# Kernel tuning notes

Measured on AMD Instinct MI355X. Metric: run time of the kernel, lower is better.

The kernel has to match this reference:

```python
import jax, jax.numpy as jnp
from jax import lax
import numpy as np

B, W, D = 32, 256, 512      # batch, input_window, d_model == feature_size
NHID = W // 2               # GAT hidden per head = 128
NHEADS = 4
ALPHA = 0.1                 # LeakyReLU slope (GAT default)
NEG = -1e9                  # masked-softmax fill


def conv1d(x, w, b):
    # x: [B, C, L], w: [O, I, K=3], 'same' padding, stride 1
    y = lax.conv_general_dilated(x, w, (1,), 'SAME', dimension_numbers=('NCH', 'OIH', 'NCH'))
    return y + b[None, :, None]


def gat_heads(h, adj, Wt, bb, ai, ai_b, aj, aj_b):
    # h: [B, N, F_in], adj: [B, N, N]; vectorized over NHEADS heads
    Wh = jnp.einsum('bnf,hof->bhno', h, Wt) + bb[None, :, None, :]   # [B,H,N,NHID]
    e1 = jnp.einsum('bhno,ho->bhn', Wh, ai) + ai_b[None, :, None]
    e2 = jnp.einsum('bhno,ho->bhn', Wh, aj) + aj_b[None, :, None]
    e = jax.nn.leaky_relu(e1[..., :, None] + e2[..., None, :], ALPHA)  # [B,H,N,N]
    att = jax.nn.softmax(jnp.where(adj[:, None] > 0, e, NEG), axis=-1)
    return jnp.einsum('bhnm,bhmo->bhno', att, Wh)


def gat_out(h, adj, Wt, bb, ai, ai_b, aj, aj_b):
    # h: [B, N, NHEADS*NHID] -> [B, N, W]
    Wh = h @ Wt.T + bb
    e1 = Wh @ ai + ai_b
    e2 = Wh @ aj + aj_b
    e = jax.nn.leaky_relu(e1[:, :, None] + e2[:, None, :], ALPHA)
    att = jax.nn.softmax(jnp.where(adj > 0, e, NEG), axis=-1)
    return jnp.einsum('bnm,bmo->bno', att, Wh)


def setup_inputs() -> dict:
    key = jax.random.key(0)
    ks = jax.random.split(key, 16)
    f32 = jnp.float32
    def xu(k, shape, fan_in):
        return jax.random.normal(k, shape, f32) * (1.414 / np.sqrt(fan_in))
    return {
        'x': jax.random.normal(ks[0], (B, W, D), f32),
        'qW': xu(ks[1], (D, D, 3), 3 * D), 'qb': jnp.zeros((D,), f32),
        'kW': xu(ks[2], (D, D, 3), 3 * D), 'kb': jnp.zeros((D,), f32),
        'vW': xu(ks[3], (D, D, 3), 3 * D), 'vb': jnp.zeros((D,), f32),
        'head_W': xu(ks[4], (NHEADS, NHID, W), W), 'head_b': jnp.zeros((NHEADS, NHID), f32),
        'head_ai': xu(ks[5], (NHEADS, NHID), NHID), 'head_ai_b': jnp.zeros((NHEADS,), f32),
        'head_aj': xu(ks[6], (NHEADS, NHID), NHID), 'head_aj_b': jnp.zeros((NHEADS,), f32),
        'out_W': xu(ks[7], (W, NHEADS * NHID), NHEADS * NHID), 'out_b': jnp.zeros((W,), f32),
        'out_ai': xu(ks[8], (W,), W), 'out_ai_b': jnp.zeros((), f32),
        'out_aj': xu(ks[9], (W,), W), 'out_aj_b': jnp.zeros((), f32),
        'proj_W': xu(ks[10], (D, D), D), 'proj_b': jnp.zeros((D,), f32),
    }


def reference(x, qW, qb, kW, kb, vW, vb,
              head_W, head_b, head_ai, head_ai_b, head_aj, head_aj_b,
              out_W, out_b, out_ai, out_ai_b, out_aj, out_aj_b,
              proj_W, proj_b):
    b, w, f = x.shape
    xt = jnp.transpose(x, (0, 2, 1))                 # [B, D, W]
    q = conv1d(xt, qW, qb)
    k = conv1d(xt, kW, kb)
    v = conv1d(xt, vW, vb)
    scale = 1.0 / jnp.sqrt(jnp.asarray(f, x.dtype))  # q.shape[-2] == d_model
    adj = jax.nn.sigmoid(jnp.einsum('bdw,bew->bde', q, k) * scale)  # [B, D, D]
    # GAT: nodes = feature dims (N=D), node features = window (W); dropout skipped (eval)
    hh = jax.nn.elu(gat_heads(v, adj, head_W, head_b, head_ai, head_ai_b, head_aj, head_aj_b))
    hcat = jnp.transpose(hh, (0, 2, 1, 3)).reshape(b, f, NHEADS * NHID)  # [B, D, 4*NHID]
    g = gat_out(hcat, adj, out_W, out_b, out_ai, out_ai_b, out_aj, out_aj_b)
    gat_y = jax.nn.log_softmax(jax.nn.elu(g), axis=2)  # [B, D, W]
    out = jnp.transpose(gat_y, (0, 2, 1)) @ proj_W.T + proj_b  # [B, W, D]
    return (out, adj)
```

## Files before the change

kernel.cpp:

```cpp
#include <hip/hip_runtime.h>
#include <math.h>

typedef unsigned short u16;
typedef __attribute__((ext_vector_type(8))) short short8;
typedef __attribute__((ext_vector_type(4))) float f32x4;

#define BB 32
#define WW 256
#define DD 512
#define NHEADS 4
#define NHID 128

__device__ __forceinline__ u16 f2bf(float f) {
  union { float f; unsigned int i; } x; x.f = f;
  unsigned int i = x.i;
  i += 0x7fffu + ((i >> 16) & 1u);
  return (u16)(i >> 16);
}
__device__ __forceinline__ float bf2f(u16 u) {
  union { float f; unsigned int i; } x; x.i = ((unsigned int)u) << 16; return x.f;
}

union BF8 { short8 v; u16 u[8]; };
union BF4 { ushort4 v; u16 u[4]; };
union F8 { float4 v4[2]; float f[8]; };

__global__ __launch_bounds__(256) void kprep_w(
    const float* __restrict__ qW, const float* __restrict__ kW, const float* __restrict__ vW,
    u16* __restrict__ Wt)
{
  int idx = blockIdx.x*256 + threadIdx.x;
  if (idx >= 3*DD*DD) return;
  int c = idx >> 18;
  int oi = idx & (DD*DD - 1);
  int i = oi & (DD-1);
  int o = oi >> 9;
  const float* W = (c==0) ? qW : (c==1) ? kW : vW;
  float w0 = W[oi*3+0], w1 = W[oi*3+1], w2 = W[oi*3+2];
  Wt[((size_t)(c*3+0)*DD + o)*DD + i] = f2bf(w0);
  Wt[((size_t)(c*3+1)*DD + o)*DD + i] = f2bf(w1);
  Wt[((size_t)(c*3+2)*DD + o)*DD + i] = f2bf(w2);
}

__global__ __launch_bounds__(256) void kcvt(const float* __restrict__ s, u16* __restrict__ d, int n) {
  int i = blockIdx.x*256 + threadIdx.x;
  if (i < n) d[i] = f2bf(s[i]);
}

__global__ __launch_bounds__(256) void kprep_a(
    const float* __restrict__ hW, const float* __restrict__ hai, const float* __restrict__ haib,
    const float* __restrict__ haj, const float* __restrict__ hajb,
    const float* __restrict__ hb,
    const float* __restrict__ oW, const float* __restrict__ oai, const float* __restrict__ oaib,
    const float* __restrict__ oaj, const float* __restrict__ oajb,
    const float* __restrict__ ob,
    float* __restrict__ ahat_i, float* __restrict__ ahat_j,
    float* __restrict__ oahat_i, float* __restrict__ oahat_j,
    float* __restrict__ cvec)
{
  int idx = blockIdx.x*256 + threadIdx.x;
  if (idx < 1024) {
    int h = idx >> 8, f = idx & 255;
    float s = 0.f;
    for (int o = 0; o < NHID; ++o) s += hW[((size_t)h*NHID + o)*WW + f] * hai[h*NHID + o];
    ahat_i[idx] = s;
  } else if (idx < 2048) {
    int t = idx - 1024; int h = t >> 8, f = t & 255;
    float s = 0.f;
    for (int o = 0; o < NHID; ++o) s += hW[((size_t)h*NHID + o)*WW + f] * haj[h*NHID + o];
    ahat_j[t] = s;
  } else if (idx < 2560) {
    int f = idx - 2048;
    float s = 0.f;
    for (int o = 0; o < WW; ++o) s += oW[(size_t)o*DD + f] * oai[o];
    oahat_i[f] = s;
  } else if (idx < 3072) {
    int f = idx - 2560;
    float s = 0.f;
    for (int o = 0; o < WW; ++o) s += oW[(size_t)o*DD + f] * oaj[o];
    oahat_j[f] = s;
  } else if (idx < 3082) {
    int t = idx - 3072;
    if (t < 4) {
      float s = 0.f;
      for (int o = 0; o < NHID; ++o) s += hb[t*NHID + o]*hai[t*NHID + o];
      cvec[t] = s + haib[t];
    } else if (t < 8) {
      int h = t - 4; float s = 0.f;
      for (int o = 0; o < NHID; ++o) s += hb[h*NHID + o]*haj[h*NHID + o];
      cvec[t] = s + hajb[h];
    } else if (t == 8) {
      float s = 0.f;
      for (int o = 0; o < WW; ++o) s += ob[o]*oai[o];
      cvec[8] = s + oaib[0];
    } else {
      float s = 0.f;
      for (int o = 0; o < WW; ++o) s += ob[o]*oaj[o];
      cvec[9] = s + oajb[0];
    }
  }
}

__global__ __launch_bounds__(256) void kprep_x(
    const float* __restrict__ x, int zb, int nrow8, u16* __restrict__ xpad)
{
  int idx8 = blockIdx.x*256 + threadIdx.x;
  if (idx8 >= nrow8) return;
  int i8 = idx8 & 63;
  int rowg = idx8 >> 6;
  int z = rowg / 258, r = rowg - z*258;
  int t = r - 1;
  BF8 o8;
  if (t >= 0 && t < WW) {
    const float* src = x + ((size_t)(zb+z)*WW + t)*DD + i8*8;
    float4 v0 = *reinterpret_cast<const float4*>(src);
    float4 v1 = *reinterpret_cast<const float4*>(src + 4);
    o8.u[0]=f2bf(v0.x); o8.u[1]=f2bf(v0.y); o8.u[2]=f2bf(v0.z); o8.u[3]=f2bf(v0.w);
    o8.u[4]=f2bf(v1.x); o8.u[5]=f2bf(v1.y); o8.u[6]=f2bf(v1.z); o8.u[7]=f2bf(v1.w);
  } else {
    #pragma unroll
    for (int j = 0; j < 8; ++j) o8.u[j] = 0;
  }
  *reinterpret_cast<short8*>(xpad + (size_t)rowg*DD + i8*8) = o8.v;
}

__global__ __launch_bounds__(256) void kexp2(
    const float* __restrict__ e2, float* __restrict__ M2,
    float* __restrict__ E2p, float* __restrict__ E2n)
{
  __shared__ float s4[4];
  const int zh = blockIdx.x, tid = threadIdx.x;
  float v0 = e2[(size_t)zh*DD + tid], v1 = e2[(size_t)zh*DD + 256 + tid];
  float m = fmaxf(v0, v1);
  #pragma unroll
  for (int off=32; off>=1; off>>=1) m = fmaxf(m, __shfl_xor(m, off));
  if ((tid & 63) == 0) s4[tid >> 6] = m;
  __syncthreads();
  m = fmaxf(fmaxf(s4[0], s4[1]), fmaxf(s4[2], s4[3]));
  if (tid == 0) M2[zh] = m;
  E2p[(size_t)zh*DD + tid]       = expf(v0 - m);
  E2p[(size_t)zh*DD + 256 + tid] = expf(v1 - m);
  E2n[(size_t)zh*DD + tid]       = expf(0.1f*(v0 - m));
  E2n[(size_t)zh*DD + 256 + tid] = expf(0.1f*(v1 - m));
}

__global__ __launch_bounds__(256) void k1_mfma(
    const u16* __restrict__ xpad, const u16* __restrict__ Wt,
    const float* __restrict__ qb, const float* __restrict__ kb, const float* __restrict__ vb,
    u16* __restrict__ qbf, u16* __restrict__ kbf, u16* __restrict__ vbf)
{
  __shared__ u16 bt[2][130*64];
  const int tid = threadIdx.x;
  const int w  = tid >> 6;
  const int l  = tid & 63;
  const int ln = l & 15;
  const int kg = l >> 4;
  const int og = blockIdx.x * 64 + w * 16;
  const int t0 = blockIdx.y * 128;
  const int z  = blockIdx.z;

  const u16* A0 = Wt + (size_t)(og + ln)*DD + kg*8;
  const u16* Xb = xpad + ((size_t)z*258 + t0)*DD;

  f32x4 acc[3][8];
  #pragma unroll
  for (int c=0;c<3;++c)
    #pragma unroll
    for (int ts=0;ts<8;++ts) acc[c][ts] = (f32x4){0.f,0.f,0.f,0.f};

  short8 ArP[9], ArQ[9];
  short8 sg0, sg1, sg2, sg3, sg4;
  const int ccw = tid & 7;
  const int rs = tid >> 3;

#define K1_LOADX(i0v) do { \
    sg0 = *reinterpret_cast<const short8*>(Xb + (size_t)rs*DD + (i0v) + ccw*8); \
    sg1 = *reinterpret_cast<const short8*>(Xb + (size_t)(rs+32)*DD + (i0v) + ccw*8); \
    sg2 = *reinterpret_cast<const short8*>(Xb + (size_t)(rs+64)*DD + (i0v) + ccw*8); \
    sg3 = *reinterpret_cast<const short8*>(Xb + (size_t)(rs+96)*DD + (i0v) + ccw*8); \
    if (tid < 16) sg4 = *reinterpret_cast<const short8*>(Xb + (size_t)(rs+128)*DD + (i0v) + ccw*8); \
  } while(0)

#define K1_WRITEX(bufv) do { \
    *reinterpret_cast<short8*>(&bt[bufv][rs*64 + ((ccw^(rs&7))<<3)]) = sg0; \
    *reinterpret_cast<short8*>(&bt[bufv][(rs+32)*64 + ((ccw^((rs+32)&7))<<3)]) = sg1; \
    *reinterpret_cast<short8*>(&bt[bufv][(rs+64)*64 + ((ccw^((rs+64)&7))<<3)]) = sg2; \
    *reinterpret_cast<short8*>(&bt[bufv][(rs+96)*64 + ((ccw^((rs+96)&7))<<3)]) = sg3; \
    if (tid < 16) *reinterpret_cast<short8*>(&bt[bufv][(rs+128)*64 + ((ccw^((rs+128)&7))<<3)]) = sg4; \
  } while(0)

#define K1_LOADA(Abuf, i0v, khv) do { \
    _Pragma("unroll") \
    for (int c = 0; c < 3; ++c) { \
      _Pragma("unroll") \
      for (int tap = 0; tap < 3; ++tap) \
        Abuf[c*3+tap] = *reinterpret_cast<const short8*>(A0 + (size_t)(c*3+tap)*DD*DD + (i0v) + (khv)*32); \
    } \
  } while(0)

#define K1_MFMAS(Abuf, khv) do { \
    _Pragma("unroll") \
    for (int tap = 0; tap < 3; ++tap) { \
      _Pragma("unroll") \
      for (int ts = 0; ts < 8; ++ts) { \
        int row = ts*16 + ln + tap; \
        short8 bfr = *reinterpret_cast<const short8*>(&bt[cur][row*64 + ((((khv)*4+kg) ^ (row&7))<<3)]); \
        acc[0][ts] = __builtin_amdgcn_mfma_f32_16x16x32_bf16(Abuf[0*3+tap], bfr, acc[0][ts], 0,0,0); \
        acc[1][ts] = __builtin_amdgcn_mfma_f32_16x16x32_bf16(Abuf[1*3+tap], bfr, acc[1][ts], 0,0,0); \
        acc[2][ts] = __builtin_amdgcn_mfma_f32_16x16x32_bf16(Abuf[2*3+tap], bfr, acc[2][ts], 0,0,0); \
      } \
    } \
  } while(0)

  K1_LOADX(0);
  K1_LOADA(ArP, 0, 0);
  K1_WRITEX(0);
  __syncthreads();

  int cur = 0;
  #pragma unroll 1
  for (int p = 0; p < 8; ++p) {
    const int i0 = p*64;
    if (p < 7) K1_LOADX(i0 + 64);
    K1_LOADA(ArQ, i0, 1);
    K1_MFMAS(ArP, 0);
    const int i0n = (p < 7) ? i0 + 64 : 0;
    K1_LOADA(ArP, i0n, 0);
    K1_MFMAS(ArQ, 1);
    if (p < 7) {
      K1_WRITEX(cur ^ 1);
      __syncthreads();
      cur ^= 1;
    }
  }

#undef K1_LOADX
#undef K1_WRITEX
#undef K1_LOADA
#undef K1_MFMAS

  #pragma unroll
  for (int ts=0; ts<8; ++ts) {
    int tg = t0 + ts*16 + ln;
    #pragma unroll
    for (int r=0;r<4;++r) {
      int o = og + kg*4 + r;
      size_t oi = (size_t)(z*DD + o)*WW + tg;
      qbf[oi] = f2bf(acc[0][ts][r] + qb[o]);
      kbf[oi] = f2bf(acc[1][ts][r] + kb[o]);
      vbf[oi] = f2bf(acc[2][ts][r] + vb[o]);
    }
  }
}

__global__ __launch_bounds__(256) void k2_adj(
    const u16* __restrict__ qbf, const u16* __restrict__ kbf, int zb, float* __restrict__ adjo)
{
  __shared__ u16 bp[2][64*64];
  const int tid = threadIdx.x;
  const int w = tid >> 6, l = tid & 63, ln = l & 15, kg = l >> 4;
  const int d0 = blockIdx.x*64 + w*16;
  const int e0 = blockIdx.y*64;
  const int z  = blockIdx.z;
  const int sc = tid & 7, sr = tid >> 3;
  const int sp = sc ^ (sr & 7);
  const int sp2 = sc ^ ((sr+32) & 7);
  const u16* B0 = kbf + (size_t)(z*DD + e0)*WW;
  const u16* Asrc = qbf + (size_t)(z*DD + d0 + ln)*WW + kg*8;

  f32x4 acc[4];
  #pragma unroll
  for (int es=0;es<4;++es) acc[es] = (f32x4){0.f,0.f,0.f,0.f};
  short8 aP0, aP1, aQ0, aQ1, sg0, sg1;

  sg0 = *reinterpret_cast<const short8*>(B0 + (size_t)sr*WW + sc*8);
  sg1 = *reinterpret_cast<const short8*>(B0 + (size_t)(sr+32)*WW + sc*8);
  aP0 = *reinterpret_cast<const short8*>(Asrc);
  aP1 = *reinterpret_cast<const short8*>(Asrc + 32);
  *reinterpret_cast<short8*>(&bp[0][sr*64 + sp*8]) = sg0;
  *reinterpret_cast<short8*>(&bp[0][(sr+32)*64 + sp2*8]) = sg1;
  __syncthreads();

  int cur = 0;
  #pragma unroll 1
  for (int s = 0; s < 4; ++s) {
    const int fn = (s+1)*64;
    if (s < 3) {
      sg0 = *reinterpret_cast<const short8*>(B0 + (size_t)sr*WW + fn + sc*8);
      sg1 = *reinterpret_cast<const short8*>(B0 + (size_t)(sr+32)*WW + fn + sc*8);
      aQ0 = *reinterpret_cast<const short8*>(Asrc + fn);
      aQ1 = *reinterpret_cast<const short8*>(Asrc + fn + 32);
    }
    #pragma unroll
    for (int es = 0; es < 4; ++es) {
      int row = es*16 + ln;
      short8 b0 = *reinterpret_cast<const short8*>(&bp[cur][row*64 + ((kg ^ (row&7))<<3)]);
      acc[es] = __builtin_amdgcn_mfma_f32_16x16x32_bf16(aP0, b0, acc[es], 0,0,0);
      short8 b1 = *reinterpret_cast<const short8*>(&bp[cur][row*64 + (((4+kg) ^ (row&7))<<3)]);
      acc[es] = __builtin_amdgcn_mfma_f32_16x16x32_bf16(aP1, b1, acc[es], 0,0,0);
    }
    if (s < 3) {
      *reinterpret_cast<short8*>(&bp[cur^1][sr*64 + sp*8]) = sg0;
      *reinterpret_cast<short8*>(&bp[cur^1][(sr+32)*64 + sp2*8]) = sg1;
      __syncthreads();
      cur ^= 1;
      aP0 = aQ0; aP1 = aQ1;
    }
  }
  const float scale = 0.044194173824159216f;
  #pragma unroll
  for (int es=0; es<4; ++es)
    #pragma unroll
    for (int r=0; r<4; ++r) {
      float sig = 1.f/(1.f + expf(-acc[es][r]*scale));
      adjo[((size_t)(zb+z)*DD + d0 + kg*4 + r)*DD + e0 + es*16 + ln] = sig;
    }
}

__global__ __launch_bounds__(256) void k3_wh(
    const u16* __restrict__ vbf, const u16* __restrict__ hWbf, const float* __restrict__ hb,
    u16* __restrict__ Whtbf)
{
  __shared__ u16 bp[2][64*64];
  const int tid = threadIdx.x;
  const int w = tid >> 6, l = tid & 63, ln = l & 15, kg = l >> 4;
  const int n0 = blockIdx.x*64 + w*16;
  const int o0 = blockIdx.y*64;
  const int zh = blockIdx.z, z = zh >> 2, h = zh & 3;
  const int sc = tid & 7, sr = tid >> 3;
  const int sp = sc ^ (sr & 7);
  const int sp2 = sc ^ ((sr+32) & 7);
  const u16* B0 = hWbf + (size_t)(h*NHID + o0)*WW;
  const u16* Asrc = vbf + (size_t)(z*DD + n0 + ln)*WW + kg*8;

  f32x4 acc[4];
  #pragma unroll
  for (int os=0;os<4;++os) acc[os] = (f32x4){0.f,0.f,0.f,0.f};
  short8 aP0, aP1, aQ0, aQ1, sg0, sg1;

  sg0 = *reinterpret_cast<const short8*>(B0 + (size_t)sr*WW + sc*8);
  sg1 = *reinterpret_cast<const short8*>(B0 + (size_t)(sr+32)*WW + sc*8);
  aP0 = *reinterpret_cast<const short8*>(Asrc);
  aP1 = *reinterpret_cast<const short8*>(Asrc + 32);
  *reinterpret_cast<short8*>(&bp[0][sr*64 + sp*8]) = sg0;
  *reinterpret_cast<short8*>(&bp[0][(sr+32)*64 + sp2*8]) = sg1;
  __syncthreads();

  int cur = 0;
  #pragma unroll 1
  for (int s = 0; s < 4; ++s) {
    const int fn = (s+1)*64;
    if (s < 3) {
      sg0 = *reinterpret_cast<const short8*>(B0 + (size_t)sr*WW + fn + sc*8);
      sg1 = *reinterpret_cast<const short8*>(B0 + (size_t)(sr+32)*WW + fn + sc*8);
      aQ0 = *reinterpret_cast<const short8*>(Asrc + fn);
      aQ1 = *reinterpret_cast<const short8*>(Asrc + fn + 32);
    }
    #pragma unroll
    for (int os = 0; os < 4; ++os) {
      int row = os*16 + ln;
      short8 b0 = *reinterpret_cast<const short8*>(&bp[cur][row*64 + ((kg ^ (row&7))<<3)]);
      acc[os] = __builtin_amdgcn_mfma_f32_16x16x32_bf16(aP0, b0, acc[os], 0,0,0);
      short8 b1 = *reinterpret_cast<const short8*>(&bp[cur][row*64 + (((4+kg) ^ (row&7))<<3)]);
      acc[os] = __builtin_amdgcn_mfma_f32_16x16x32_bf16(aP1, b1, acc[os], 0,0,0);
    }
    if (s < 3) {
      *reinterpret_cast<short8*>(&bp[cur^1][sr*64 + sp*8]) = sg0;
      *reinterpret_cast<short8*>(&bp[cur^1][(sr+32)*64 + sp2*8]) = sg1;
      __syncthreads();
      cur ^= 1;
      aP0 = aQ0; aP1 = aQ1;
    }
  }
  #pragma unroll
  for (int os=0; os<4; ++os)
    #pragma unroll
    for (int r=0; r<4; ++r) {
      int o = o0 + os*16 + ln;
      int n = n0 + kg*4 + r;
      Whtbf[((size_t)zh*NHID + o)*DD + n] = f2bf(acc[os][r] + hb[h*NHID + o]);
    }
}

__global__ __launch_bounds__(256) void k4_eheads(
    const u16* __restrict__ vbf,
    const float* __restrict__ ahat_i, const float* __restrict__ ahat_j,
    const float* __restrict__ cvec,
    float* __restrict__ e1, float* __restrict__ e2)
{
  int row = blockIdx.x*4 + (threadIdx.x >> 6);
  int lane = threadIdx.x & 63;
  int zh = row >> 9, n = row & 511;
  int z = zh >> 2, h = zh & 3;
  BF4 v4; v4.v = *reinterpret_cast<const ushort4*>(vbf + ((size_t)(z*DD + n))*WW + lane*4);
  const float* aif = ahat_i + h*WW + lane*4;
  const float* ajf = ahat_j + h*WW + lane*4;
  float a1 = 0.f, a2 = 0.f;
  #pragma unroll
  for (int j = 0; j < 4; ++j) {
    float vf = bf2f(v4.u[j]);
    a1 += vf * aif[j];
    a2 += vf * ajf[j];
  }
  #pragma unroll
  for (int off = 32; off >= 1; off >>= 1) { a1 += __shfl_xor(a1, off); a2 += __shfl_xor(a2, off); }
  if (lane == 0) { e1[row] = a1 + cvec[h]; e2[row] = a2 + cvec[4+h]; }
}

__device__ __forceinline__ int attsw(int c, int row) {
  return c ^ ((c >> 3) & 7) ^ (row & 7);
}

#define PA_LD(Ea,Pa,Na,jcv) do { int j0=(jcv)*8; \
    Ea.v4[0]=*reinterpret_cast<const float4*>(e2r+j0); Ea.v4[1]=*reinterpret_cast<const float4*>(e2r+j0+4); \
    Pa.v4[0]=*reinterpret_cast<const float4*>(Epr+j0); Pa.v4[1]=*reinterpret_cast<const float4*>(Epr+j0+4); \
    Na.v4[0]=*reinterpret_cast<const float4*>(Enr+j0); Na.v4[1]=*reinterpret_cast<const float4*>(Enr+j0+4); } while(0)
#define PA_PROC(att, Ea,Pa,Na,jcv) do { BF8 pk; \
    _Pragma("unroll") \
    for (int jj=0;jj<8;++jj){ float p=(Ea.f[jj]>thr)?Ap*Pa.f[jj]:An*Na.f[jj]; lsum+=p; pk.u[jj]=f2bf(p);} \
    int c=qd*8+(jcv); *reinterpret_cast<short8*>(&att[r*512+attsw(c,r)*8])=pk.v; } while(0)

__global__ __launch_bounds__(512) void k5_attn(
    const float* __restrict__ e1h, const float* __restrict__ e2h,
    const float* __restrict__ M2h, const float* __restrict__ E2p, const float* __restrict__ E2n,
    const u16* __restrict__ Whtbf, u16* __restrict__ hcatbf, int nzh)
{
  __shared__ u16 att[64*512];
  __shared__ float inv_lds[64];
  const int orig = blockIdx.x;
  const int xcd = orig & 7;
  const int k = orig >> 3;
  const int nb = k & 7;
  const int zh = xcd * (nzh >> 3) + (k >> 3);
  const int z = zh >> 2, h = zh & 3;
  const int n0 = nb*64;
  const int tid = threadIdx.x;

  const int r = tid >> 3, qd = tid & 7;
  const float e1n = e1h[(size_t)zh*DD + n0 + r];
  const float M2 = M2h[zh];
  const float s = e1n + M2;
  const float mx = (s > 0.f) ? s : 0.1f*s;
  const float Ap = expf(s - mx);
  const float An = expf(0.1f*s - mx);
  const float thr = -e1n;
  const float* e2r = e2h + (size_t)zh*DD + qd*64;
  const float* Epr = E2p + (size_t)zh*DD + qd*64;
  const float* Enr = E2n + (size_t)zh*DD + qd*64;
  float lsum = 0.f;
  {
    F8 e2a,epa,ena, e2b,epb,enb;
    PA_LD(e2a,epa,ena,0);
    PA_LD(e2b,epb,enb,1);
    PA_PROC(att, e2a,epa,ena,0);
    PA_LD(e2a,epa,ena,2);
    PA_PROC(att, e2b,epb,enb,1);
    PA_LD(e2b,epb,enb,3);
    PA_PROC(att, e2a,epa,ena,2);
    PA_LD(e2a,epa,ena,4);
    PA_PROC(att, e2b,epb,enb,3);
    PA_LD(e2b,epb,enb,5);
    PA_PROC(att, e2a,epa,ena,4);
    PA_LD(e2a,epa,ena,6);
    PA_PROC(att, e2b,epb,enb,5);
    PA_LD(e2b,epb,enb,7);
    PA_PROC(att, e2a,epa,ena,6);
    PA_PROC(att, e2b,epb,enb,7);
  }
  lsum += __shfl_xor(lsum, 1);
  lsum += __shfl_xor(lsum, 2);
  lsum += __shfl_xor(lsum, 4);
  if ((tid & 7) == 0) inv_lds[r] = 1.f / lsum;
  __syncthreads();

  const int w = tid >> 6, l = tid & 63, ln = l & 15, kg = l >> 4;
  const u16* B0 = Whtbf + ((size_t)zh*NHID + w*16 + ln)*DD + kg*8;
  f32x4 acc[4];
  #pragma unroll
  for (int ns=0; ns<4; ++ns) acc[ns] = (f32x4){0,0,0,0};

  short8 Pb,Qb,Rb,Sb;
  short8 af0[4], af1[4];
#define K5_LDB(R0,kkv) do { int kc = ((kkv) < 16) ? (kkv) : 0; \
    R0 = *reinterpret_cast<const short8*>(B0 + (size_t)kc*32); } while(0)
#define K5_AFLD(AF,kkv) do { int kc = ((kkv) < 16) ? (kkv) : 0; \
    _Pragma("unroll") \
    for (int ns = 0; ns < 4; ++ns) { int row = ns*16 + ln; int c = kc*4 + kg; \
      AF[ns] = *reinterpret_cast<const short8*>(&att[row*512 + attsw(c,row)*8]); } } while(0)
#define K5_MM(AF,R0) do { \
    _Pragma("unroll") \
    for (int ns = 0; ns < 4; ++ns) \
      acc[ns] = __builtin_amdgcn_mfma_f32_16x16x32_bf16(AF[ns], R0, acc[ns], 0,0,0); } while(0)

  K5_LDB(Pb,0); K5_LDB(Qb,1); K5_LDB(Rb,2);
  K5_AFLD(af0,0);
  #pragma unroll 1
  for (int kk = 0; kk < 16; kk += 4) {
    K5_LDB(Sb,kk+3); K5_AFLD(af1,kk+1); K5_MM(af0,Pb);
    K5_LDB(Pb,kk+4); K5_AFLD(af0,kk+2); K5_MM(af1,Qb);
    K5_LDB(Qb,kk+5); K5_AFLD(af1,kk+3); K5_MM(af0,Rb);
    K5_LDB(Rb,kk+6); K5_AFLD(af0,kk+4); K5_MM(af1,Sb);
  }
#undef K5_LDB
#undef K5_AFLD
#undef K5_MM

  #pragma unroll
  for (int ns = 0; ns < 4; ++ns)
    #pragma unroll
    for (int rr = 0; rr < 4; ++rr) {
      int n = ns*16 + kg*4 + rr;
      float inv = inv_lds[n];
      float sv = acc[ns][rr] * inv;
      sv = (sv > 0.f) ? sv : expm1f(sv);
      hcatbf[((size_t)z*DD + n0 + n)*DD + h*NHID + w*16 + ln] = f2bf(sv);
    }
}

__global__ __launch_bounds__(256) void k6_wh2(
    const u16* __restrict__ hcatbf, const u16* __restrict__ oWbf, const float* __restrict__ ob,
    u16* __restrict__ Wh2tbf)
{
  __shared__ u16 bp[2][64*64];
  const int tid = threadIdx.x;
  const int w = tid >> 6, l = tid & 63, ln = l & 15, kg = l >> 4;
  const int n0 = blockIdx.x*64 + w*16;
  const int o0 = blockIdx.y*64;
  const int z  = blockIdx.z;
  const int sc = tid & 7, sr = tid >> 3;
  const int sp = sc ^ (sr & 7);
  const int sp2 = sc ^ ((sr+32) & 7);
  const u16* B0 = oWbf + (size_t)o0*DD;
  const u16* Asrc = hcatbf + (size_t)(z*DD + n0 + ln)*DD + kg*8;

  f32x4 acc[4];
  #pragma unroll
  for (int os=0;os<4;++os) acc[os] = (f32x4){0.f,0.f,0.f,0.f};
  short8 aP0, aP1, aQ0, aQ1, sg0, sg1;

  sg0 = *reinterpret_cast<const short8*>(B0 + (size_t)sr*DD + sc*8);
  sg1 = *reinterpret_cast<const short8*>(B0 + (size_t)(sr+32)*DD + sc*8);
  aP0 = *reinterpret_cast<const short8*>(Asrc);
  aP1 = *reinterpret_cast<const short8*>(Asrc + 32);
  *reinterpret_cast<short8*>(&bp[0][sr*64 + sp*8]) = sg0;
  *reinterpret_cast<short8*>(&bp[0][(sr+32)*64 + sp2*8]) = sg1;
  __syncthreads();

  int cur = 0;
  #pragma unroll 1
  for (int s = 0; s < 8; ++s) {
    const int fn = (s+1)*64;
    if (s < 7) {
      sg0 = *reinterpret_cast<const short8*>(B0 + (size_t)sr*DD + fn + sc*8);
      sg1 = *reinterpret_cast<const short8*>(B0 + (size_t)(sr+32)*DD + fn + sc*8);
      aQ0 = *reinterpret_cast<const short8*>(Asrc + fn);
      aQ1 = *reinterpret_cast<const short8*>(Asrc + fn + 32);
    }
    #pragma unroll
    for (int os = 0; os < 4; ++os) {
      int row = os*16 + ln;
      short8 b0 = *reinterpret_cast<const short8*>(&bp[cur][row*64 + ((kg ^ (row&7))<<3)]);
      acc[os] = __builtin_amdgcn_mfma_f32_16x16x32_bf16(aP0, b0, acc[os], 0,0,0);
      short8 b1 = *reinterpret_cast<const short8*>(&bp[cur][row*64 + (((4+kg) ^ (row&7))<<3)]);
      acc[os] = __builtin_amdgcn_mfma_f32_16x16x32_bf16(aP1, b1, acc[os], 0,0,0);
    }
    if (s < 7) {
      *reinterpret_cast<short8*>(&bp[cur^1][sr*64 + sp*8]) = sg0;
      *reinterpret_cast<short8*>(&bp[cur^1][(sr+32)*64 + sp2*8]) = sg1;
      __syncthreads();
      cur ^= 1;
      aP0 = aQ0; aP1 = aQ1;
    }
  }
  #pragma unroll
  for (int os=0; os<4; ++os)
    #pragma unroll
    for (int r=0; r<4; ++r) {
      int o = o0 + os*16 + ln;
      int n = n0 + kg*4 + r;
      Wh2tbf[((size_t)z*WW + o)*DD + n] = f2bf(acc[os][r] + ob[o]);
    }
}

__global__ __launch_bounds__(256) void k7_eout(
    const u16* __restrict__ hcatbf,
    const float* __restrict__ oahat_i, const float* __restrict__ oahat_j,
    const float* __restrict__ cvec,
    float* __restrict__ e1, float* __restrict__ e2)
{
  int row = blockIdx.x*4 + (threadIdx.x >> 6);
  int lane = threadIdx.x & 63;
  BF8 v8; v8.v = *reinterpret_cast<const short8*>(hcatbf + (size_t)row*DD + lane*8);
  float a1 = 0.f, a2 = 0.f;
  #pragma unroll
  for (int j = 0; j < 8; ++j) {
    float vf = bf2f(v8.u[j]);
    a1 += vf * oahat_i[lane*8 + j];
    a2 += vf * oahat_j[lane*8 + j];
  }
  #pragma unroll
  for (int off = 32; off >= 1; off >>= 1) { a1 += __shfl_xor(a1, off); a2 += __shfl_xor(a2, off); }
  if (lane == 0) { e1[row] = a1 + cvec[8]; e2[row] = a2 + cvec[9]; }
}

__global__ __launch_bounds__(512) void k8_pv(
    const float* __restrict__ e1o, const float* __restrict__ e2o,
    const float* __restrict__ M2o, const float* __restrict__ E2p, const float* __restrict__ E2n,
    const u16* __restrict__ Wh2tbf, float* __restrict__ g, int CBv)
{
  __shared__ u16 att[64*512];
  __shared__ float inv_lds[64];
  const int orig = blockIdx.x;
  int nb, z, oh;
  if (CBv >= 8) {
    int xcd = orig & 7;
    int k = orig >> 3;
    nb = k & 7;
    int rest = k >> 3;
    oh = rest & 1;
    z = xcd * (CBv >> 3) + (rest >> 1);
  } else {
    nb = orig & 7;
    int k = orig >> 3;
    z = k >> 1;
    oh = k & 1;
  }
  const int n0 = nb*64;
  const int tid = threadIdx.x;

  const int r = tid >> 3, qd = tid & 7;
  const float e1n = e1o[(size_t)z*DD + n0 + r];
  const float M2 = M2o[z];
  const float s = e1n + M2;
  const float mx = (s > 0.f) ? s : 0.1f*s;
  const float Ap = expf(s - mx);
  const float An = expf(0.1f*s - mx);
  const float thr = -e1n;
  const float* e2r = e2o + (size_t)z*DD + qd*64;
  const float* Epr = E2p + (size_t)z*DD + qd*64;
  const float* Enr = E2n + (size_t)z*DD + qd*64;
  float lsum = 0.f;
  {
    F8 e2a,epa,ena, e2b,epb,enb;
    PA_LD(e2a,epa,ena,0);
    PA_LD(e2b,epb,enb,1);
    PA_PROC(att, e2a,epa,ena,0);
    PA_LD(e2a,epa,ena,2);
    PA_PROC(att, e2b,epb,enb,1);
    PA_LD(e2b,epb,enb,3);
    PA_PROC(att, e2a,epa,ena,2);
    PA_LD(e2a,epa,ena,4);
    PA_PROC(att, e2b,epb,enb,3);
    PA_LD(e2b,epb,enb,5);
    PA_PROC(att, e2a,epa,ena,4);
    PA_LD(e2a,epa,ena,6);
    PA_PROC(att, e2b,epb,enb,5);
    PA_LD(e2b,epb,enb,7);
    PA_PROC(att, e2a,epa,ena,6);
    PA_PROC(att, e2b,epb,enb,7);
  }
  lsum += __shfl_xor(lsum, 1);
  lsum += __shfl_xor(lsum, 2);
  lsum += __shfl_xor(lsum, 4);
  if ((tid & 7) == 0) inv_lds[r] = 1.f / lsum;
  __syncthreads();

  const int w = tid >> 6, l = tid & 63, ln = l & 15, kg = l >> 4;
  const u16* B0 = Wh2tbf + ((size_t)z*WW + oh*128 + w*16 + ln)*DD + kg*8;
  f32x4 acc[4];
  #pragma unroll
  for (int ns=0; ns<4; ++ns) acc[ns] = (f32x4){0,0,0,0};

  short8 Pb,Qb,Rb,Sb;
  short8 af0[4], af1[4];
#define K8_LDB(R0,kkv) do { int kc = ((kkv) < 16) ? (kkv) : 0; \
    R0 = *reinterpret_cast<const short8*>(B0 + (size_t)kc*32); } while(0)
#define K8_AFLD(AF,kkv) do { int kc = ((kkv) < 16) ? (kkv) : 0; \
    _Pragma("unroll") \
    for (int ns = 0; ns < 4; ++ns) { int row = ns*16 + ln; int c = kc*4 + kg; \
      AF[ns] = *reinterpret_cast<const short8*>(&att[row*512 + attsw(c,row)*8]); } } while(0)
#define K8_MM(AF,R0) do { \
    _Pragma("unroll") \
    for (int ns = 0; ns < 4; ++ns) \
      acc[ns] = __builtin_amdgcn_mfma_f32_16x16x32_bf16(AF[ns], R0, acc[ns], 0,0,0); } while(0)

  K8_LDB(Pb,0); K8_LDB(Qb,1); K8_LDB(Rb,2);
  K8_AFLD(af0,0);
  #pragma unroll 1
  for (int kk = 0; kk < 16; kk += 4) {
    K8_LDB(Sb,kk+3); K8_AFLD(af1,kk+1); K8_MM(af0,Pb);
    K8_LDB(Pb,kk+4); K8_AFLD(af0,kk+2); K8_MM(af1,Qb);
    K8_LDB(Qb,kk+5); K8_AFLD(af1,kk+3); K8_MM(af0,Rb);
    K8_LDB(Rb,kk+6); K8_AFLD(af0,kk+4); K8_MM(af1,Sb);
  }
#undef K8_LDB
#undef K8_AFLD
#undef K8_MM

  #pragma unroll
  for (int ns = 0; ns < 4; ++ns)
    #pragma unroll
    for (int rr = 0; rr < 4; ++rr) {
      int n = ns*16 + kg*4 + rr;
      float inv = inv_lds[n];
      float val = acc[ns][rr] * inv;
      val = (val > 0.f) ? val : expm1f(val);
      g[((size_t)z*DD + n0 + n)*WW + oh*128 + w*16 + ln] = val;
    }
}

__global__ __launch_bounds__(256) void k8_lsm(
    const float* __restrict__ g, u16* __restrict__ gatybf)
{
  int row = blockIdx.x*4 + (threadIdx.x >> 6);
  int lane = threadIdx.x & 63;
  const float* gr = g + (size_t)row*WW;
  float v0 = gr[lane], v1 = gr[lane+64], v2 = gr[lane+128], v3 = gr[lane+192];
  float mx = fmaxf(fmaxf(v0,v1), fmaxf(v2,v3));
  #pragma unroll
  for (int off = 32; off >= 1; off >>= 1) mx = fmaxf(mx, __shfl_xor(mx, off));
  float sm = expf(v0-mx) + expf(v1-mx) + expf(v2-mx) + expf(v3-mx);
  #pragma unroll
  for (int off = 32; off >= 1; off >>= 1) sm += __shfl_xor(sm, off);
  float lg = mx + logf(sm);
  u16* go = gatybf + (size_t)row*WW;
  go[lane]     = f2bf(v0 - lg);
  go[lane+64]  = f2bf(v1 - lg);
  go[lane+128] = f2bf(v2 - lg);
  go[lane+192] = f2bf(v3 - lg);
}

__global__ __launch_bounds__(256) void k9_proj(
    const u16* __restrict__ gatybf, const u16* __restrict__ pWbf, const float* __restrict__ pb,
    int zb, float* __restrict__ out0)
{
  __shared__ u16 gt[64*40];
  const int t0 = blockIdx.x*64, d0 = blockIdx.y*64, z = blockIdx.z;
  const int tid = threadIdx.x;
  const int w = tid >> 6, l = tid & 63, ln = l & 15, kg = l >> 4;
  const int el = tid >> 3, t8 = tid & 7;
  f32x4 acc[4];
  #pragma unroll
  for (int os=0;os<4;++os) acc[os] = (f32x4){0.f,0.f,0.f,0.f};
  for (int e0 = 0; e0 < DD; e0 += 32) {
    __syncthreads();
    BF8 g8;
    g8.v = *reinterpret_cast<const short8*>(gatybf + ((size_t)z*DD + e0 + el)*WW + t0 + t8*8);
    #pragma unroll
    for (int j = 0; j < 8; ++j) gt[(t8*8 + j)*40 + el] = g8.u[j];
    __syncthreads();
    short8 a = *reinterpret_cast<const short8*>(&gt[(w*16 + ln)*40 + kg*8]);
    #pragma unroll
    for (int os = 0; os < 4; ++os) {
      short8 b = *reinterpret_cast<const short8*>(pWbf + (size_t)(d0 + os*16 + ln)*DD + e0 + kg*8);
      acc[os] = __builtin_amdgcn_mfma_f32_16x16x32_bf16(a, b, acc[os], 0,0,0);
    }
  }
  #pragma unroll
  for (int os=0; os<4; ++os)
    #pragma unroll
    for (int rr=0; rr<4; ++rr) {
      int t = t0 + w*16 + kg*4 + rr;
      int d = d0 + os*16 + ln;
      out0[((size_t)(zb+z)*WW + t)*DD + d] = acc[os][rr] + pb[d];
    }
}

extern "C" void kernel_launch(void* const* d_in, const int* in_sizes, int n_in,
                              void* d_out, int out_size, void* d_ws, size_t ws_size,
                              hipStream_t stream)
{
  const float* x   = (const float*)d_in[0];
  const float* qW  = (const float*)d_in[1];
  const float* qb  = (const float*)d_in[2];
  const float* kW  = (const float*)d_in[3];
  const float* kb  = (const float*)d_in[4];
  const float* vW  = (const float*)d_in[5];
  const float* vb  = (const float*)d_in[6];
  const float* hW  = (const float*)d_in[7];
  const float* hb  = (const float*)d_in[8];
  const float* hai = (const float*)d_in[9];
  const float* haib= (const float*)d_in[10];
  const float* haj = (const float*)d_in[11];
  const float* hajb= (const float*)d_in[12];
  const float* oW  = (const float*)d_in[13];
  const float* ob  = (const float*)d_in[14];
  const float* oai = (const float*)d_in[15];
  const float* oaib= (const float*)d_in[16];
  const float* oaj = (const float*)d_in[17];
  const float* oajb= (const float*)d_in[18];
  const float* pW  = (const float*)d_in[19];
  const float* pb  = (const float*)d_in[20];

  float* out0 = (float*)d_out;
  float* adjo = out0 + (size_t)BB*WW*DD;

  float* ws      = (float*)d_ws;
  u16*   Wt      = (u16*)(ws + 0);
  u16*   hWbf    = (u16*)(ws + 1179648);
  u16*   oWbf    = (u16*)(ws + 1245184);
  u16*   pWbf    = (u16*)(ws + 1310720);
  float* ahat_i  = ws + 1441792;
  float* ahat_j  = ws + 1442816;
  float* oahat_i = ws + 1443840;
  float* oahat_j = ws + 1444352;
  float* cvec    = ws + 1444864;
  float* e1h     = ws + 1444880;
  float* e2h     = ws + 1510416;
  float* e1o     = ws + 1575952;
  float* e2o     = ws + 1592336;
  float* M2h     = ws + 1608720;
  float* E2hp    = ws + 1608848;
  float* E2hn    = ws + 1674384;
  float* M2o     = ws + 1739920;
  float* E2op    = ws + 1739952;
  float* E2on    = ws + 1756336;
  const size_t X0 = 1772720;

  int CB = 4;
  {
    const int cand[3] = {32, 16, 8};
    for (int i = 0; i < 3; ++i) {
      size_t need = (X0 + (size_t)cand[i]*393728) * 4;
      if (need <= ws_size) { CB = cand[i]; break; }
    }
  }

  u16* xpad   = (u16*)(ws + X0);
  u16* vbf    = (u16*)(ws + X0 + (size_t)CB*66048);
  u16* qbf    = (u16*)(ws + X0 + (size_t)CB*131584);
  u16* kbf    = (u16*)(ws + X0 + (size_t)CB*197120);
  u16* Whtbf  = (u16*)(ws + X0 + (size_t)CB*262656);
  u16*   hcatbf = (u16*)(ws + X0);
  float* g      = (float*)(ws + X0);
  u16*   gatybf = (u16*)(ws + X0 + (size_t)CB*131584);
  u16*   Wh2tbf = (u16*)(ws + X0 + (size_t)CB*197120);

  kprep_w<<<dim3((3*DD*DD + 255)/256), 256, 0, stream>>>(qW, kW, vW, Wt);
  kcvt<<<dim3((NHEADS*NHID*WW + 255)/256), 256, 0, stream>>>(hW, hWbf, NHEADS*NHID*WW);
  kcvt<<<dim3((WW*DD + 255)/256), 256, 0, stream>>>(oW, oWbf, WW*DD);
  kcvt<<<dim3((DD*DD + 255)/256), 256, 0, stream>>>(pW, pWbf, DD*DD);
  kprep_a<<<dim3(13), 256, 0, stream>>>(hW, hai, haib, haj, hajb, hb,
                                        oW, oai, oaib, oaj, oajb, ob,
                                        ahat_i, ahat_j, oahat_i, oahat_j, cvec);

  for (int zb = 0; zb < BB; zb += CB) {
    int nrow8 = CB*258*64;
    kprep_x  <<<dim3((nrow8 + 255)/256), 256, 0, stream>>>(x, zb, nrow8, xpad);
    k1_mfma  <<<dim3(DD/64, WW/128, CB), 256, 0, stream>>>(xpad, Wt, qb, kb, vb, qbf, kbf, vbf);
    k2_adj   <<<dim3(DD/64, DD/64, CB), 256, 0, stream>>>(qbf, kbf, zb, adjo);
    k3_wh    <<<dim3(DD/64, NHID/64, CB*NHEADS), 256, 0, stream>>>(vbf, hWbf, hb, Whtbf);
    k4_eheads<<<dim3(CB*NHEADS*DD/4), 256, 0, stream>>>(vbf, ahat_i, ahat_j, cvec, e1h, e2h);
    kexp2    <<<dim3(CB*NHEADS), 256, 0, stream>>>(e2h, M2h, E2hp, E2hn);
    k5_attn  <<<dim3(32*CB), 512, 0, stream>>>(e1h, e2h, M2h, E2hp, E2hn, Whtbf, hcatbf, CB*NHEADS);
    k6_wh2   <<<dim3(DD/64, WW/64, CB), 256, 0, stream>>>(hcatbf, oWbf, ob, Wh2tbf);
    k7_eout  <<<dim3(CB*DD/4), 256, 0, stream>>>(hcatbf, oahat_i, oahat_j, cvec, e1o, e2o);
    kexp2    <<<dim3(CB), 256, 0, stream>>>(e2o, M2o, E2op, E2on);
    k8_pv    <<<dim3(16*CB), 512, 0, stream>>>(e1o, e2o, M2o, E2op, E2on, Wh2tbf, g, CB);
    k8_lsm   <<<dim3(CB*128), 256, 0, stream>>>(g, gatybf);
    k9_proj  <<<dim3(WW/64, DD/64, CB), 256, 0, stream>>>(gatybf, pWbf, pb, zb, out0);
  }
}
```

Measured before the change: 311.2 us.

## Fuse output-GAT PV matmul with ELU and log-softmax into one kernel

Each k8 block now computes all 256 output columns for its 64 rows instead of splitting them into two halves. This lets the row-wise log-softmax run in-block through LDS reductions and write bf16 gat_y directly. It removes the fp32 g round trip to global memory and the separate k8_lsm launch, and no longer recomputes the attention softmax twice per row tile. In exchange the grid is halved, which lowers parallelism, and the kernel carries more accumulator registers and extra block-wide syncs.

```diff
diff --git a/kernel.cpp b/kernel.cpp
--- a/kernel.cpp
+++ b/kernel.cpp
@@ -603,27 +603,23 @@
   if (lane == 0) { e1[row] = a1 + cvec[8]; e2[row] = a2 + cvec[9]; }
 }
 
-__global__ __launch_bounds__(512) void k8_pv(
+__global__ __launch_bounds__(512) void k8_fused(
     const float* __restrict__ e1o, const float* __restrict__ e2o,
     const float* __restrict__ M2o, const float* __restrict__ E2p, const float* __restrict__ E2n,
-    const u16* __restrict__ Wh2tbf, float* __restrict__ g, int CBv)
+    const u16* __restrict__ Wh2tbf, u16* __restrict__ gatybf, int CBv)
 {
   __shared__ u16 att[64*512];
   __shared__ float inv_lds[64];
   const int orig = blockIdx.x;
-  int nb, z, oh;
+  int nb, z;
   if (CBv >= 8) {
     int xcd = orig & 7;
     int k = orig >> 3;
     nb = k & 7;
-    int rest = k >> 3;
-    oh = rest & 1;
-    z = xcd * (CBv >> 3) + (rest >> 1);
+    z = xcd * (CBv >> 3) + (k >> 3);
   } else {
     nb = orig & 7;
-    int k = orig >> 3;
-    z = k >> 1;
-    oh = k & 1;
+    z = orig >> 3;
   }
   const int n0 = nb*64;
   const int tid = threadIdx.x;
@@ -632,9 +628,9 @@
   const float e1n = e1o[(size_t)z*DD + n0 + r];
   const float M2 = M2o[z];
   const float s = e1n + M2;
-  const float mx = (s > 0.f) ? s : 0.1f*s;
-  const float Ap = expf(s - mx);
-  const float An = expf(0.1f*s - mx);
+  const float mxA = (s > 0.f) ? s : 0.1f*s;
+  const float Ap = expf(s - mxA);
+  const float An = expf(0.1f*s - mxA);
   const float thr = -e1n;
   const float* e2r = e2o + (size_t)z*DD + qd*64;
   const float* Epr = E2p + (size_t)z*DD + qd*64;
@@ -666,68 +662,107 @@
   __syncthreads();
 
   const int w = tid >> 6, l = tid & 63, ln = l & 15, kg = l >> 4;
-  const u16* B0 = Wh2tbf + ((size_t)z*WW + oh*128 + w*16 + ln)*DD + kg*8;
-  f32x4 acc[4];
-  #pragma unroll
-  for (int ns=0; ns<4; ++ns) acc[ns] = (f32x4){0,0,0,0};
-
-  short8 Pb,Qb,Rb,Sb;
+  const u16* B0 = Wh2tbf + ((size_t)z*WW + w*16 + ln)*DD + kg*8;
+  f32x4 acc[4][2];
+  #pragma unroll
+  for (int ns=0; ns<4; ++ns) { acc[ns][0] = (f32x4){0,0,0,0}; acc[ns][1] = (f32x4){0,0,0,0}; }
+
+  short8 Pb0,Pb1,Qb0,Qb1;
   short8 af0[4], af1[4];
-#define K8_LDB(R0,kkv) do { int kc = ((kkv) < 16) ? (kkv) : 0; \
-    R0 = *reinterpret_cast<const short8*>(B0 + (size_t)kc*32); } while(0)
+#define K8_LDB(R0,R1,kkv) do { int kc = ((kkv) < 16) ? (kkv) : 0; \
+    R0 = *reinterpret_cast<const short8*>(B0 + (size_t)kc*32); \
+    R1 = *reinterpret_cast<const short8*>(B0 + (size_t)128*DD + (size_t)kc*32); } while(0)
 #define K8_AFLD(AF,kkv) do { int kc = ((kkv) < 16) ? (kkv) : 0; \
     _Pragma("unroll") \
     for (int ns = 0; ns < 4; ++ns) { int row = ns*16 + ln; int c = kc*4 + kg; \
       AF[ns] = *reinterpret_cast<const short8*>(&att[row*512 + attsw(c,row)*8]); } } while(0)
-#define K8_MM(AF,R0) do { \
+#define K8_MM(AF,R0,R1) do { \
     _Pragma("unroll") \
-    for (int ns = 0; ns < 4; ++ns) \
-      acc[ns] = __builtin_amdgcn_mfma_f32_16x16x32_bf16(AF[ns], R0, acc[ns], 0,0,0); } while(0)
-
-  K8_LDB(Pb,0); K8_LDB(Qb,1); K8_LDB(Rb,2);
+    for (int ns = 0; ns < 4; ++ns) { \
+      acc[ns][0] = __builtin_amdgcn_mfma_f32_16x16x32_bf16(AF[ns], R0, acc[ns][0], 0,0,0); \
+      acc[ns][1] = __builtin_amdgcn_mfma_f32_16x16x32_bf16(AF[ns], R1, acc[ns][1], 0,0,0); \
+    } } while(0)
+
+  K8_LDB(Pb0,Pb1,0);
   K8_AFLD(af0,0);
   #pragma unroll 1
-  for (int kk = 0; kk < 16; kk += 4) {
-    K8_LDB(Sb,kk+3); K8_AFLD(af1,kk+1); K8_MM(af0,Pb);
-    K8_LDB(Pb,kk+4); K8_AFLD(af0,kk+2); K8_MM(af1,Qb);
-    K8_LDB(Qb,kk+5); K8_AFLD(af1,kk+3); K8_MM(af0,Rb);
-    K8_LDB(Rb,kk+6); K8_AFLD(af0,kk+4); K8_MM(af1,Sb);
+  for (int kk = 0; kk < 16; kk += 2) {
+    K8_LDB(Qb0,Qb1,kk+1); K8_AFLD(af1,kk+1); K8_MM(af0,Pb0,Pb1);
+    K8_LDB(Pb0,Pb1,kk+2); K8_AFLD(af0,kk+2); K8_MM(af1,Qb0,Qb1);
   }
 #undef K8_LDB
 #undef K8_AFLD
 #undef K8_MM
 
-  #pragma unroll
-  for (int ns = 0; ns < 4; ++ns)
+  __syncthreads();
+  float* red = (float*)att;
+  float inv_r[4];
+  #pragma unroll
+  for (int ns=0; ns<4; ++ns) inv_r[ns] = 0.f;
+
+  #pragma unroll
+  for (int ns = 0; ns < 4; ++ns) {
     #pragma unroll
     for (int rr = 0; rr < 4; ++rr) {
       int n = ns*16 + kg*4 + rr;
       float inv = inv_lds[n];
-      float val = acc[ns][rr] * inv;
-      val = (val > 0.f) ? val : expm1f(val);
-      g[((size_t)z*DD + n0 + n)*WW + oh*128 + w*16 + ln] = val;
-    }
-}
-
-__global__ __launch_bounds__(256) void k8_lsm(
-    const float* __restrict__ g, u16* __restrict__ gatybf)
-{
-  int row = blockIdx.x*4 + (threadIdx.x >> 6);
-  int lane = threadIdx.x & 63;
-  const float* gr = g + (size_t)row*WW;
-  float v0 = gr[lane], v1 = gr[lane+64], v2 = gr[lane+128], v3 = gr[lane+192];
-  float mx = fmaxf(fmaxf(v0,v1), fmaxf(v2,v3));
-  #pragma unroll
-  for (int off = 32; off >= 1; off >>= 1) mx = fmaxf(mx, __shfl_xor(mx, off));
-  float sm = expf(v0-mx) + expf(v1-mx) + expf(v2-mx) + expf(v3-mx);
-  #pragma unroll
-  for (int off = 32; off >= 1; off >>= 1) sm += __shfl_xor(sm, off);
-  float lg = mx + logf(sm);
-  u16* go = gatybf + (size_t)row*WW;
-  go[lane]     = f2bf(v0 - lg);
-  go[lane+64]  = f2bf(v1 - lg);
-  go[lane+128] = f2bf(v2 - lg);
-  go[lane+192] = f2bf(v3 - lg);
+      float v0 = acc[ns][0][rr] * inv; v0 = (v0 > 0.f) ? v0 : expm1f(v0);
+      float v1 = acc[ns][1][rr] * inv; v1 = (v1 > 0.f) ? v1 : expm1f(v1);
+      float m = fmaxf(v0, v1);
+      m = fmaxf(m, __shfl_xor(m, 1));
+      m = fmaxf(m, __shfl_xor(m, 2));
+      m = fmaxf(m, __shfl_xor(m, 4));
+      m = fmaxf(m, __shfl_xor(m, 8));
+      if (ln == 0) red[n*8 + w] = m;
+    }
+  }
+  __syncthreads();
+  if (tid < 64) {
+    float m = red[tid*8];
+    #pragma unroll
+    for (int j = 1; j < 8; ++j) m = fmaxf(m, red[tid*8 + j]);
+    red[1024 + tid] = m;
+  }
+  __syncthreads();
+  #pragma unroll
+  for (int ns = 0; ns < 4; ++ns) {
+    #pragma unroll
+    for (int rr = 0; rr < 4; ++rr) {
+      int n = ns*16 + kg*4 + rr;
+      float inv = inv_lds[n];
+      float mxn = red[1024 + n];
+      float v0 = acc[ns][0][rr] * inv; v0 = (v0 > 0.f) ? v0 : expm1f(v0);
+      float v1 = acc[ns][1][rr] * inv; v1 = (v1 > 0.f) ? v1 : expm1f(v1);
+      float sm = expf(v0 - mxn) + expf(v1 - mxn);
+      sm += __shfl_xor(sm, 1);
+      sm += __shfl_xor(sm, 2);
+      sm += __shfl_xor(sm, 4);
+      sm += __shfl_xor(sm, 8);
+      if (ln == 0) red[512 + n*8 + w] = sm;
+    }
+  }
+  __syncthreads();
+  if (tid < 64) {
+    float sm = 0.f;
+    #pragma unroll
+    for (int j = 0; j < 8; ++j) sm += red[512 + tid*8 + j];
+    red[1088 + tid] = red[1024 + tid] + logf(sm);
+  }
+  __syncthreads();
+  #pragma unroll
+  for (int ns = 0; ns < 4; ++ns) {
+    #pragma unroll
+    for (int rr = 0; rr < 4; ++rr) {
+      int n = ns*16 + kg*4 + rr;
+      float inv = inv_lds[n];
+      float lg = red[1088 + n];
+      float v0 = acc[ns][0][rr] * inv; v0 = (v0 > 0.f) ? v0 : expm1f(v0);
+      float v1 = acc[ns][1][rr] * inv; v1 = (v1 > 0.f) ? v1 : expm1f(v1);
+      size_t base = ((size_t)z*DD + n0 + n)*WW;
+      gatybf[base + w*16 + ln]       = f2bf(v0 - lg);
+      gatybf[base + 128 + w*16 + ln] = f2bf(v1 - lg);
+    }
+  }
 }
 
 __global__ __launch_bounds__(256) void k9_proj(
@@ -832,7 +867,6 @@
   u16* kbf    = (u16*)(ws + X0 + (size_t)CB*197120);
   u16* Whtbf  = (u16*)(ws + X0 + (size_t)CB*262656);
   u16*   hcatbf = (u16*)(ws + X0);
-  float* g      = (float*)(ws + X0);
   u16*   gatybf = (u16*)(ws + X0 + (size_t)CB*131584);
   u16*   Wh2tbf = (u16*)(ws + X0 + (size_t)CB*197120);
 
@@ -856,8 +890,7 @@
     k6_wh2   <<<dim3(DD/64, WW/64, CB), 256, 0, stream>>>(hcatbf, oWbf, ob, Wh2tbf);
     k7_eout  <<<dim3(CB*DD/4), 256, 0, stream>>>(hcatbf, oahat_i, oahat_j, cvec, e1o, e2o);
     kexp2    <<<dim3(CB), 256, 0, stream>>>(e2o, M2o, E2op, E2on);
-    k8_pv    <<<dim3(16*CB), 512, 0, stream>>>(e1o, e2o, M2o, E2op, E2on, Wh2tbf, g, CB);
-    k8_lsm   <<<dim3(CB*128), 256, 0, stream>>>(g, gatybf);
+    k8_fused <<<dim3(8*CB), 512, 0, stream>>>(e1o, e2o, M2o, E2op, E2on, Wh2tbf, gatybf, CB);
     k9_proj  <<<dim3(WW/64, DD/64, CB), 256, 0, stream>>>(gatybf, pWbf, pb, zb, out0);
   }
 }
```

New measurement: 303.7 us. -2.4%, faster.
